# Kernel optimization log

Hardware: AMD Instinct MI355X
Metric: run time of the kernel (lower is better)

## Reference

```python
import math
import jax, jax.numpy as jnp
import numpy as np

B, N, DIM, H = 2, 4096, 1024, 16
DH = DIM // H
LEVELS = int(math.log2(N))
SCALE = 1.0 / math.sqrt(DH)


def build_lookup_table(seq_len):
    """Replicates build_hierarchical_index_lookup_table (numpy, static)."""
    levels = int(math.log2(seq_len))
    total_nodes = 2 * seq_len - 1
    max_valid = total_nodes - 2
    idx = np.full((seq_len, levels), -1, dtype=np.int32)
    cm = np.zeros((seq_len, levels), dtype=bool)
    for n in range(seq_len):
        nc = n
        for l in range(levels):
            if l == 0:
                pair = nc
                nn = nc ^ 1
            else:
                pair = nc // 2 + seq_len
                nn = pair ^ 1  # (nc//2 + seq_len) ^ 1 per Python precedence
            if nn > max_valid:
                break
            if pair < nn:
                cm[n, l] = True  # neighbor is to the right -> causally masked
            idx[n, l] = nn
            nc = nn
    return idx, cm


def setup_inputs() -> dict:
    key = jax.random.key(0)
    ks = jax.random.split(key, 12)
    w = lambda k: (jax.random.normal(k, (DIM, DIM), dtype=jnp.float32) * 0.02)
    idx_np, cm_np = build_lookup_table(N)
    return {
        "x": jax.random.normal(ks[0], (B, N, DIM), dtype=jnp.float32),
        "Wq_y": w(ks[1]), "Wk_y": w(ks[2]), "Wv_y": w(ks[3]),
        "Wo_y": w(ks[4]), "bo_y": jnp.zeros((DIM,), jnp.float32),
        "Wq_x": w(ks[5]), "Wk_x": w(ks[6]), "Wv_x": w(ks[7]),
        "Wo_x": w(ks[8]), "bo_x": jnp.zeros((DIM,), jnp.float32),
        "idx_map": jnp.asarray(idx_np, dtype=jnp.int32),       # [N, LEVELS]
        "causal_mask": jnp.asarray(cm_np, dtype=jnp.bool_),    # [N, LEVELS]
    }


def _heads(t):
    b, n, _ = t.shape
    return t.reshape(b, n, H, DH)


def _forward(x, Wq_y, Wk_y, Wv_y, Wo_y, bo_y, Wq_x, Wk_x, Wv_x, Wo_x, bo_x,
             idx_map, causal_mask):
    # ---- stage 1: build parent nodes level by level (online 2-child softmax merge)
    nodes = [x]  # leaves: [B, N, DIM]; parents appended level by level
    cur = x
    for _ in range(LEVELS):
        pre = 0.5 * (cur[:, 0::2] + cur[:, 1::2])     # parent query source [B,P,DIM]
        q = _heads(pre @ Wq_y)                        # [B,P,H,DH]
        k = _heads(cur @ Wk_y)                        # [B,C,H,DH]
        v = _heads(cur @ Wv_y)
        s0 = jnp.einsum('bphd,bphd->bph', q, k[:, 0::2]) * SCALE
        s1 = jnp.einsum('bphd,bphd->bph', q, k[:, 1::2]) * SCALE
        m = jnp.maximum(s0, s1)
        e0 = jnp.exp(s0 - m)
        e1 = jnp.exp(s1 - m)
        denom = e0 + e1 + 1e-9
        parent = ((e0 / denom)[..., None] * v[:, 0::2]
                  + (e1 / denom)[..., None] * v[:, 1::2])   # [B,P,H,DH]
        bp, pp = parent.shape[0], parent.shape[1]
        parent = parent.reshape(bp, pp, DIM) @ Wo_y + bo_y
        nodes.append(parent)
        cur = parent
    h_all = jnp.concatenate(nodes, axis=1)            # [B, 2N-1, DIM]

    # ---- stage 2: fused multi-level gather attention over self + neighbors
    Q = _heads(x @ Wq_x)                              # leaf queries [B,N,H,DH]
    K_all = _heads(h_all @ Wk_x)                      # [B,2N-1,H,DH]
    V_all = _heads(h_all @ Wv_x)

    k_cross = jnp.take(K_all, idx_map, axis=1)        # [B,N,LEVELS,H,DH]
    v_cross = jnp.take(V_all, idx_map, axis=1)

    s_self = jnp.einsum('bnhd,bnhd->bnh', Q, K_all[:, :N]) * SCALE   # [B,N,H]
    s_cross = jnp.einsum('bnhd,bnlhd->bnhl', Q, k_cross) * SCALE     # [B,N,H,L]
    neg_inf = jnp.float32(-jnp.inf)
    s_cross = jnp.where(causal_mask[None, :, None, :], neg_inf, s_cross)

    scores = jnp.concatenate([s_self[..., None], s_cross], axis=-1)  # [B,N,H,L+1]
    w = jax.nn.softmax(scores, axis=-1)
    out = (w[..., 0:1] * V_all[:, :N]
           + jnp.einsum('bnhl,bnlhd->bnhd', w[..., 1:], v_cross))    # [B,N,H,DH]
    return out.reshape(B, N, DIM) @ Wo_x + bo_x


def reference(x, Wq_y, Wk_y, Wv_y, Wo_y, bo_y, Wq_x, Wk_x, Wv_x, Wo_x, bo_x,
              idx_map, causal_mask):
    return _forward(x, Wq_y, Wk_y, Wv_y, Wo_y, bo_y,
                    Wq_x, Wk_x, Wv_x, Wo_x, bo_x, idx_map, causal_mask)
```

## Files before the change

kernel.cpp:

```cpp
#include <hip/hip_runtime.h>
#include <stdint.h>

#define H_NODES 8191
#define NN 4096
#define DIMC 1024

typedef __bf16 bf16x8 __attribute__((ext_vector_type(8)));
typedef float f32x4 __attribute__((ext_vector_type(4)));

__device__ __forceinline__ float b2f(ushort u) {
  union { uint32_t i; float f; } x; x.i = ((uint32_t)u) << 16; return x.f;
}
__device__ __forceinline__ ushort f2b(float f) {
  union { float f; uint32_t i; } x; x.f = f;
  uint32_t r = x.i + 0x7FFFu + ((x.i >> 16) & 1u);
  return (ushort)(r >> 16);
}
__device__ __forceinline__ void load16f(const ushort* p, float* f) {
  const uint32_t* w = (const uint32_t*)p;
  #pragma unroll
  for (int i = 0; i < 8; ++i) {
    uint32_t v = w[i];
    f[2 * i]     = b2f((ushort)(v & 0xffff));
    f[2 * i + 1] = b2f((ushort)(v >> 16));
  }
}
__device__ __forceinline__ void store16b(ushort* p, const float* f) {
  uint32_t w[8];
  #pragma unroll
  for (int i = 0; i < 8; ++i)
    w[i] = (uint32_t)f2b(f[2 * i]) | ((uint32_t)f2b(f[2 * i + 1]) << 16);
  *(uint4*)p = *(const uint4*)&w[0];
  *(uint4*)(p + 8) = *(const uint4*)&w[4];
}

struct WPtrs { const float* w[8]; };

__global__ void __launch_bounds__(256) transpose_w_k(WPtrs wp, ushort* __restrict__ dst) {
  __shared__ float t[32][33];
  const float* src = wp.w[blockIdx.z];
  int c0 = blockIdx.x * 32, r0 = blockIdx.y * 32;
  int tx = threadIdx.x, ty = threadIdx.y;
  #pragma unroll
  for (int i = ty; i < 32; i += 8)
    t[i][tx] = src[(long)(r0 + i) * DIMC + c0 + tx];
  __syncthreads();
  ushort* d = dst + (long)blockIdx.z * DIMC * DIMC;
  #pragma unroll
  for (int i = ty; i < 32; i += 8)
    d[(long)(c0 + i) * DIMC + r0 + tx] = f2b(t[tx][i]);
}

__global__ void __launch_bounds__(256) cvt_x_k(const float* __restrict__ x, ushort* __restrict__ h) {
  long t = (long)blockIdx.x * 256 + threadIdx.x;
  long i = t << 2;
  if (i >= (long)2 * NN * DIMC) return;
  long row = i >> 10;
  int col = (int)(i & 1023);
  long b = row >> 12;
  long n = row & 4095;
  float4 v = *(const float4*)(x + i);
  ushort* d = h + ((b * H_NODES + n) << 10) + col;
  uint2 pk;
  pk.x = (uint32_t)f2b(v.x) | ((uint32_t)f2b(v.y) << 16);
  pk.y = (uint32_t)f2b(v.z) | ((uint32_t)f2b(v.w) << 16);
  *(uint2*)d = pk;
}

__global__ void __launch_bounds__(256) avg_pairs_k(const ushort* __restrict__ h,
    ushort* __restrict__ pre, int P, int offL) {
  long t = (long)blockIdx.x * 256 + threadIdx.x;
  if (t >= (long)2 * P * 128) return;
  int dblk = (int)(t & 127);
  long r = t >> 7;
  int b = (r >= P) ? 1 : 0;
  int p = (int)(r - (long)b * P);
  const ushort* c = h + (((long)(b * H_NODES + offL + 2 * p)) << 10) + dblk * 8;
  const uint4 a0 = *(const uint4*)c;
  const uint4 a1 = *(const uint4*)(c + DIMC);
  const uint32_t* pa = (const uint32_t*)&a0;
  const uint32_t* pb = (const uint32_t*)&a1;
  uint32_t outw[4];
  #pragma unroll
  for (int i = 0; i < 4; ++i) {
    float x0 = b2f((ushort)(pa[i] & 0xffff)), x1 = b2f((ushort)(pa[i] >> 16));
    float y0 = b2f((ushort)(pb[i] & 0xffff)), y1 = b2f((ushort)(pb[i] >> 16));
    ushort r0 = f2b(0.5f * (x0 + y0)), r1 = f2b(0.5f * (x1 + y1));
    outw[i] = (uint32_t)r0 | ((uint32_t)r1 << 16);
  }
  *(uint4*)(pre + (((long)(b * P + p)) << 10) + dblk * 8) = *(const uint4*)outw;
}

struct GemmDesc {
  const ushort* A; long sAb;
  const ushort* Bt;
  const float* bias;
  void* C; long sCb; int ldc;
  int M; int outMode;
  int tX, tY;
};

__device__ __forceinline__ void stage_tile(const GemmDesc& d, const ushort* Ab,
    int row0, int col0, ushort* lA, ushort* lB, int kt, int wave, int lane) {
  #pragma unroll
  for (int j = 0; j < 2; ++j) {
    int s = wave * 128 + j * 64 + lane;
    int r = s >> 2;
    int g = (s & 3) ^ ((r >> 1) & 3);
    int gr = row0 + r; gr = (gr < d.M) ? gr : (d.M - 1);
    const ushort* srcA = Ab + (long)gr * DIMC + kt * 32 + g * 8;
    __builtin_amdgcn_global_load_lds(
        (const __attribute__((address_space(1))) void*)(uintptr_t)srcA,
        (__attribute__((address_space(3))) void*)(uint32_t)(uintptr_t)(lA + (wave * 128 + j * 64) * 8),
        16, 0, 0);
    const ushort* srcB = d.Bt + (long)(col0 + r) * DIMC + kt * 32 + g * 8;
    __builtin_amdgcn_global_load_lds(
        (const __attribute__((address_space(1))) void*)(uintptr_t)srcB,
        (__attribute__((address_space(3))) void*)(uint32_t)(uintptr_t)(lB + (wave * 128 + j * 64) * 8),
        16, 0, 0);
  }
}

__device__ void gemm_tile(const GemmDesc& d, int bz, int row0, int col0,
    ushort (*lA)[4096], ushort (*lB)[4096], int tid) {
  const ushort* Ab = d.A + (long)bz * d.sAb;
  int wave = tid >> 6, lane = tid & 63;
  int wr = wave >> 1, wc = wave & 1;

  f32x4 acc[4][4];
  #pragma unroll
  for (int m = 0; m < 4; ++m)
    #pragma unroll
    for (int n = 0; n < 4; ++n) acc[m][n] = (f32x4){0.f, 0.f, 0.f, 0.f};

  stage_tile(d, Ab, row0, col0, lA[0], lB[0], 0, wave, lane);
  stage_tile(d, Ab, row0, col0, lA[1], lB[1], 1, wave, lane);
  asm volatile("s_waitcnt vmcnt(4)" ::: "memory");
  __builtin_amdgcn_s_barrier();

  int rr = lane & 15, g4 = lane >> 4;
  for (int kt = 0; kt < 32; ++kt) {
    int cur = kt % 3;
    if (kt + 2 < 32)
      stage_tile(d, Ab, row0, col0, lA[(kt + 2) % 3], lB[(kt + 2) % 3], kt + 2, wave, lane);
    bf16x8 af[4], bfr[4];
    #pragma unroll
    for (int m = 0; m < 4; ++m) {
      int r = wr * 64 + m * 16 + rr;
      int slot = g4 ^ ((r >> 1) & 3);
      af[m] = *reinterpret_cast<const bf16x8*>(&lA[cur][r * 32 + slot * 8]);
    }
    #pragma unroll
    for (int n = 0; n < 4; ++n) {
      int r = wc * 64 + n * 16 + rr;
      int slot = g4 ^ ((r >> 1) & 3);
      bfr[n] = *reinterpret_cast<const bf16x8*>(&lB[cur][r * 32 + slot * 8]);
    }
    __builtin_amdgcn_s_setprio(1);
    #pragma unroll
    for (int m = 0; m < 4; ++m)
      #pragma unroll
      for (int n = 0; n < 4; ++n)
        acc[m][n] = __builtin_amdgcn_mfma_f32_16x16x32_bf16(af[m], bfr[n], acc[m][n], 0, 0, 0);
    __builtin_amdgcn_s_setprio(0);
    if (kt < 30) { asm volatile("s_waitcnt vmcnt(4)" ::: "memory"); }
    else         { asm volatile("s_waitcnt vmcnt(0)" ::: "memory"); }
    if (kt < 31) __builtin_amdgcn_s_barrier();
  }

  int rq = lane >> 4;
  #pragma unroll
  for (int n = 0; n < 4; ++n) {
    int col = col0 + wc * 64 + n * 16 + rr;
    float bv = d.bias ? d.bias[col] : 0.0f;
    #pragma unroll
    for (int m = 0; m < 4; ++m) {
      int gr0 = row0 + wr * 64 + m * 16 + rq * 4;
      #pragma unroll
      for (int r = 0; r < 4; ++r) {
        int gr = gr0 + r;
        if (gr < d.M) {
          float vv = acc[m][n][r] + bv;
          long o = (long)bz * d.sCb + (long)gr * d.ldc + col;
          if (d.outMode == 2) ((float*)d.C)[o] = vv;
          else ((ushort*)d.C)[o] = f2b(vv);
        }
      }
    }
  }
}

__global__ void __launch_bounds__(256) gemm_multi(GemmDesc d0, GemmDesc d1, int t0) {
  __shared__ __align__(16) ushort lA[3][4096];
  __shared__ __align__(16) ushort lB[3][4096];
  int t = blockIdx.x;
  const GemmDesc& d = (t < t0) ? d0 : d1;
  int u = (t < t0) ? t : t - t0;
  int per = d.tX * d.tY;
  int bz = u / per;
  int rem = u - bz * per;
  int ty = rem / d.tX;
  int tx = rem - ty * d.tX;
  gemm_tile(d, bz, tx * 128, ty * 128, lA, lB, threadIdx.x);
}

__global__ void __launch_bounds__(256) merge_y2_k(const ushort* __restrict__ q,
    const ushort* __restrict__ kv, ushort* __restrict__ outp, int P) {
  int wave = threadIdx.x >> 6, lane = threadIdx.x & 63;
  long w = (long)blockIdx.x * 4 + wave;
  if (w >= (long)2 * P) return;
  int b = (w >= P) ? 1 : 0;
  int p = (int)(w - (long)b * P);
  const ushort* qp = q + (((long)(b * P + p)) << 10) + lane * 16;
  const ushort* kvb = kv + ((long)(b * 2 * P + 2 * p)) * 2048;
  float qf[16], k0f[16], k1f[16];
  load16f(qp, qf);
  load16f(kvb + lane * 16, k0f);
  load16f(kvb + 2048 + lane * 16, k1f);
  float d0 = 0.f, d1 = 0.f;
  #pragma unroll
  for (int j = 0; j < 16; ++j) { d0 += qf[j] * k0f[j]; d1 += qf[j] * k1f[j]; }
  d0 += __shfl_xor(d0, 1); d0 += __shfl_xor(d0, 2);
  d1 += __shfl_xor(d1, 1); d1 += __shfl_xor(d1, 2);
  float s0 = d0 * 0.125f, s1 = d1 * 0.125f;
  float mm = fmaxf(s0, s1);
  float e0 = expf(s0 - mm), e1 = expf(s1 - mm);
  float inv = 1.0f / (e0 + e1 + 1e-9f);
  float w0 = e0 * inv, w1 = e1 * inv;
  float v0f[16], v1f[16], ov[16];
  load16f(kvb + 1024 + lane * 16, v0f);
  load16f(kvb + 2048 + 1024 + lane * 16, v1f);
  #pragma unroll
  for (int j = 0; j < 16; ++j) ov[j] = w0 * v0f[j] + w1 * v1f[j];
  store16b(outp + (((long)(b * P + p)) << 10) + lane * 16, ov);
}

__global__ void __launch_bounds__(256) attn_x2_k(const ushort* __restrict__ Q,
    const ushort* __restrict__ KV, ushort* __restrict__ outp) {
  int wave = threadIdx.x >> 6, lane = threadIdx.x & 63;
  long w = (long)blockIdx.x * 4 + wave;
  int n = (int)(w & 4095);
  int b = (int)(w >> 12);
  const ushort* KVb = KV + (long)b * H_NODES * 2048;
  float qf[16];
  load16f(Q + (((long)b * NN + n) << 10) + lane * 16, qf);
  int nb[13];
  nb[0] = n;
  #pragma unroll
  for (int l = 0; l < 12; ++l) nb[1 + l] = (8192 - (8192 >> l)) + ((n >> l) ^ 1);
  float s[13];
  #pragma unroll
  for (int i = 0; i < 13; ++i) {
    float kf[16];
    load16f(KVb + (long)nb[i] * 2048 + lane * 16, kf);
    float d = 0.f;
    #pragma unroll
    for (int j = 0; j < 16; ++j) d += qf[j] * kf[j];
    d += __shfl_xor(d, 1);
    d += __shfl_xor(d, 2);
    s[i] = d * 0.125f;
  }
  #pragma unroll
  for (int l = 0; l < 12; ++l)
    if (((n >> l) & 1) == 0) s[1 + l] = -__builtin_inff();
  float mm = s[0];
  #pragma unroll
  for (int i = 1; i < 13; ++i) mm = fmaxf(mm, s[i]);
  float e[13], sum = 0.f;
  #pragma unroll
  for (int i = 0; i < 13; ++i) { e[i] = expf(s[i] - mm); sum += e[i]; }
  float inv = 1.0f / sum;
  float ov[16];
  #pragma unroll
  for (int j = 0; j < 16; ++j) ov[j] = 0.f;
  #pragma unroll
  for (int i = 0; i < 13; ++i) {
    float wgt = e[i] * inv;
    float vf[16];
    load16f(KVb + (long)nb[i] * 2048 + 1024 + lane * 16, vf);
    #pragma unroll
    for (int j = 0; j < 16; ++j) ov[j] += wgt * vf[j];
  }
  store16b(outp + (((long)b * NN + n) << 10) + lane * 16, ov);
}

extern "C" void kernel_launch(void* const* d_in, const int* in_sizes, int n_in,
                              void* d_out, int out_size, void* d_ws, size_t ws_size,
                              hipStream_t stream) {
  const float* x    = (const float*)d_in[0];
  const float* Wq_y = (const float*)d_in[1];
  const float* Wk_y = (const float*)d_in[2];
  const float* Wv_y = (const float*)d_in[3];
  const float* Wo_y = (const float*)d_in[4];
  const float* bo_y = (const float*)d_in[5];
  const float* Wq_x = (const float*)d_in[6];
  const float* Wk_x = (const float*)d_in[7];
  const float* Wv_x = (const float*)d_in[8];
  const float* Wo_x = (const float*)d_in[9];
  const float* bo_x = (const float*)d_in[10];

  ushort* wt  = (ushort*)d_ws;
  ushort* h   = wt + (size_t)8 * 1024 * 1024;
  ushort* reg = h + (size_t)2 * H_NODES * DIMC;
  ushort* pre = reg;
  ushort* qb  = pre + (size_t)2 * 2048 * DIMC;
  ushort* kv1 = qb  + (size_t)2 * 2048 * DIMC;
  ushort* mrg = kv1 + (size_t)2 * 4096 * 2048;
  ushort* Qx   = reg;
  ushort* KVa  = Qx + (size_t)2 * 4096 * DIMC;
  ushort* aout = KVa + (size_t)2 * H_NODES * 2048;

  size_t need = ((size_t)8 * 1024 * 1024 + (size_t)2 * H_NODES * DIMC +
                 (size_t)2 * 4096 * DIMC + (size_t)2 * H_NODES * 2048 +
                 (size_t)2 * 4096 * DIMC) * 2;
  if (ws_size < need) return;

  WPtrs wp;
  wp.w[0] = Wq_y; wp.w[1] = Wk_y; wp.w[2] = Wv_y; wp.w[3] = Wo_y;
  wp.w[4] = Wq_x; wp.w[5] = Wk_x; wp.w[6] = Wv_x; wp.w[7] = Wo_x;
  transpose_w_k<<<dim3(32, 32, 8), dim3(32, 8), 0, stream>>>(wp, wt);
  cvt_x_k<<<8192, 256, 0, stream>>>(x, h);

  auto mkdesc = [](const ushort* A, long sAb, const ushort* Bt, const float* bias,
                   void* C, long sCb, int ldc, int M, int outMode, int tY) {
    GemmDesc d; d.A = A; d.sAb = sAb; d.Bt = Bt; d.bias = bias; d.C = C; d.sCb = sCb;
    d.ldc = ldc; d.M = M; d.outMode = outMode; d.tX = (M + 127) / 128; d.tY = tY;
    return d;
  };

  for (int l = 0; l < 12; ++l) {
    int C = NN >> l, P = C >> 1;
    int offL = 8192 - (8192 >> l);
    int offP = 8192 - (8192 >> (l + 1));
    avg_pairs_k<<<(2 * P * 128 + 255) / 256, 256, 0, stream>>>(h, pre, P, offL);
    GemmDesc dq = mkdesc(pre, (long)P * DIMC, wt, nullptr,
                         qb, (long)P * DIMC, DIMC, P, 0, 8);
    GemmDesc dkv = mkdesc(h + (long)offL * DIMC, (long)H_NODES * DIMC,
                          wt + (size_t)1 * 1024 * 1024, nullptr,
                          kv1, (long)C * 2048, 2048, C, 0, 16);
    int t0 = dq.tX * dq.tY * 2, t1 = dkv.tX * dkv.tY * 2;
    gemm_multi<<<t0 + t1, 256, 0, stream>>>(dq, dkv, t0);
    merge_y2_k<<<(2 * P + 3) / 4, 256, 0, stream>>>(qb, kv1, mrg, P);
    GemmDesc dgo = mkdesc(mrg, (long)P * DIMC, wt + (size_t)3 * 1024 * 1024, bo_y,
                          h + (long)offP * DIMC, (long)H_NODES * DIMC, DIMC, P, 1, 8);
    gemm_multi<<<dgo.tX * dgo.tY * 2, 256, 0, stream>>>(dgo, dgo, dgo.tX * dgo.tY * 2);
  }

  GemmDesc dqx = mkdesc(h, (long)H_NODES * DIMC, wt + (size_t)4 * 1024 * 1024, nullptr,
                        Qx, (long)4096 * DIMC, DIMC, 4096, 0, 8);
  GemmDesc dkva = mkdesc(h, (long)H_NODES * DIMC, wt + (size_t)5 * 1024 * 1024, nullptr,
                         KVa, (long)H_NODES * 2048, 2048, H_NODES, 0, 16);
  int t0 = dqx.tX * dqx.tY * 2, t1 = dkva.tX * dkva.tY * 2;
  gemm_multi<<<t0 + t1, 256, 0, stream>>>(dqx, dkva, t0);
  attn_x2_k<<<2048, 256, 0, stream>>>(Qx, KVa, aout);
  GemmDesc dox = mkdesc(aout, (long)4096 * DIMC, wt + (size_t)7 * 1024 * 1024, bo_x,
                        d_out, (long)4096 * DIMC, DIMC, 4096, 2, 8);
  gemm_multi<<<dox.tX * dox.tY * 2, 256, 0, stream>>>(dox, dox, dox.tX * dox.tY * 2);
}
```

Before: 784.4 us.

## Add 256x256-tile GEMM kernel with direct-to-LDS loads for large GEMMs

Adds a new 512-thread GEMM kernel that computes 256x256 output tiles. It stages A and B through global_load_lds with an XOR-swizzled LDS layout, double buffers with half-tile prefetch interleaved across four compute phases, and raises wave priority around the MFMA blocks. The kernel replaces the 128x128 path for the large tree levels and for the final Q/KV/output projections. The larger tiles are meant to raise arithmetic intensity and reduce global and LDS traffic per FLOP. In exchange they produce fewer blocks, which can underfill the CUs, and they use 128KB of LDS per block.

Result: slower. 949.0 us (+21.0%).

```diff
diff --git a/kernel.cpp b/kernel.cpp
--- a/kernel.cpp
+++ b/kernel.cpp
@@ -204,6 +204,143 @@
   gemm_tile(d, bz, tx * 128, ty * 128, lA, lB, threadIdx.x);
 }
 
+__device__ __forceinline__ void stage_half256(const ushort* gbase, int maxRow,
+    ushort* ldsbase, int tid) {
+  #pragma unroll
+  for (int L = 0; L < 2; ++L) {
+    int s = L * 512 + tid;
+    int lrow = s >> 3, b = s & 7;
+    int gb = b ^ ((lrow >> 1) & 7);
+    int er = lrow < maxRow ? lrow : maxRow - 1;
+    const ushort* src = gbase + (long)er * DIMC + gb * 8;
+    __builtin_amdgcn_global_load_lds(
+        (const __attribute__((address_space(1))) void*)(uintptr_t)src,
+        (__attribute__((address_space(3))) void*)(uint32_t)(uintptr_t)(ldsbase + s * 8),
+        16, 0, 0);
+  }
+}
+
+__global__ void __launch_bounds__(512, 2) gemm256_multi(GemmDesc d0, GemmDesc d1, int t0full) {
+  __shared__ __align__(16) ushort smem[65536];
+  int t = blockIdx.x;
+  const GemmDesc& d = (t < t0full) ? d0 : d1;
+  int u = (t < t0full) ? t : t - t0full;
+  int per = d.tX * d.tY;
+  int bz = u / per;
+  int rem = u - bz * per;
+  int ty = rem / d.tX;
+  int tx = rem - ty * d.tX;
+  int row0 = tx * 256, col0 = ty * 256;
+  const ushort* Ab = d.A + (long)bz * d.sAb;
+  const ushort* Bt = d.Bt;
+
+  int tid = threadIdx.x;
+  int wave = tid >> 6, lane = tid & 63;
+  int wm = wave >> 2, wn = wave & 3;
+  int rr = lane & 15, g = lane >> 4;
+  int qrr = (rr >> 1) & 7;
+  int pb0 = (g ^ qrr) * 8;
+  int pb1 = ((4 + g) ^ qrr) * 8;
+
+  auto stA = [&](int tile, int half) {
+    const ushort* gbp = Ab + (long)(row0 + half * 128) * DIMC + tile * 64;
+    int maxR = d.M - row0 - half * 128;
+    stage_half256(gbp, maxR, smem + (tile & 1) * 16384 + half * 8192, tid);
+  };
+  auto stB = [&](int tile, int half) {
+    const ushort* gbp = Bt + (long)(col0 + half * 128) * DIMC + tile * 64;
+    stage_half256(gbp, 1 << 28, smem + 32768 + (tile & 1) * 16384 + half * 8192, tid);
+  };
+
+  f32x4 acc[2][2][4][2];
+  #pragma unroll
+  for (int a0 = 0; a0 < 2; ++a0)
+    #pragma unroll
+    for (int a1 = 0; a1 < 2; ++a1)
+      #pragma unroll
+      for (int a2 = 0; a2 < 4; ++a2)
+        #pragma unroll
+        for (int a3 = 0; a3 < 2; ++a3)
+          acc[a0][a1][a2][a3] = (f32x4){0.f, 0.f, 0.f, 0.f};
+
+  stA(0, 0); stA(0, 1); stB(0, 0); stB(0, 1);
+  stA(1, 0); stB(1, 0);
+  asm volatile("s_waitcnt vmcnt(4)" ::: "memory");
+  __builtin_amdgcn_s_barrier();
+
+  for (int kt = 0; kt < 16; ++kt) {
+    ushort* aCur = smem + (kt & 1) * 16384;
+    ushort* bCur = smem + 32768 + (kt & 1) * 16384;
+    #pragma unroll
+    for (int ph = 0; ph < 4; ++ph) {
+      const int qm = ph >> 1, qn = ph & 1;
+      ushort* aH = aCur + qm * 8192;
+      ushort* bH = bCur + qn * 8192;
+      bf16x8 af[4][2], bfr[2][2];
+      #pragma unroll
+      for (int m = 0; m < 4; ++m) {
+        int lr = (wm * 64 + m * 16 + rr) * 64;
+        af[m][0] = *reinterpret_cast<const bf16x8*>(aH + lr + pb0);
+        af[m][1] = *reinterpret_cast<const bf16x8*>(aH + lr + pb1);
+      }
+      #pragma unroll
+      for (int n = 0; n < 2; ++n) {
+        int lr = (wn * 32 + n * 16 + rr) * 64;
+        bfr[n][0] = *reinterpret_cast<const bf16x8*>(bH + lr + pb0);
+        bfr[n][1] = *reinterpret_cast<const bf16x8*>(bH + lr + pb1);
+      }
+      if (ph == 0 && kt + 1 < 16) stA(kt + 1, 1);
+      if (ph == 1 && kt + 1 < 16) stB(kt + 1, 1);
+      if (ph == 2 && kt + 2 < 16) stA(kt + 2, 0);
+      if (ph == 3 && kt + 2 < 16) stB(kt + 2, 0);
+      asm volatile("" ::: "memory");
+      __builtin_amdgcn_s_barrier();
+      asm volatile("s_waitcnt lgkmcnt(0)" ::: "memory");
+      __builtin_amdgcn_s_setprio(1);
+      #pragma unroll
+      for (int m = 0; m < 4; ++m)
+        #pragma unroll
+        for (int n = 0; n < 2; ++n)
+          #pragma unroll
+          for (int ks = 0; ks < 2; ++ks)
+            acc[qm][qn][m][n] = __builtin_amdgcn_mfma_f32_16x16x32_bf16(
+                af[m][ks], bfr[n][ks], acc[qm][qn][m][n], 0, 0, 0);
+      __builtin_amdgcn_s_setprio(0);
+      if (ph == 3) {
+        if (kt + 2 < 16) { asm volatile("s_waitcnt vmcnt(4)" ::: "memory"); }
+        else             { asm volatile("s_waitcnt vmcnt(0)" ::: "memory"); }
+      }
+      asm volatile("" ::: "memory");
+      __builtin_amdgcn_s_barrier();
+    }
+  }
+
+  int rq = lane >> 4;
+  #pragma unroll
+  for (int qn = 0; qn < 2; ++qn)
+    #pragma unroll
+    for (int n = 0; n < 2; ++n) {
+      int col = col0 + qn * 128 + wn * 32 + n * 16 + rr;
+      float bv = d.bias ? d.bias[col] : 0.0f;
+      #pragma unroll
+      for (int qm = 0; qm < 2; ++qm)
+        #pragma unroll
+        for (int m = 0; m < 4; ++m) {
+          int gr0 = row0 + qm * 128 + wm * 64 + m * 16 + rq * 4;
+          #pragma unroll
+          for (int r = 0; r < 4; ++r) {
+            int gr = gr0 + r;
+            if (gr < d.M) {
+              float vv = acc[qm][qn][m][n][r] + bv;
+              long o = (long)bz * d.sCb + (long)gr * d.ldc + col;
+              if (d.outMode == 2) ((float*)d.C)[o] = vv;
+              else ((ushort*)d.C)[o] = f2b(vv);
+            }
+          }
+        }
+    }
+}
+
 __global__ void __launch_bounds__(256) merge_y2_k(const ushort* __restrict__ q,
     const ushort* __restrict__ kv, ushort* __restrict__ outp, int P) {
   int wave = threadIdx.x >> 6, lane = threadIdx.x & 63;
@@ -321,10 +458,16 @@
   transpose_w_k<<<dim3(32, 32, 8), dim3(32, 8), 0, stream>>>(wp, wt);
   cvt_x_k<<<8192, 256, 0, stream>>>(x, h);
 
-  auto mkdesc = [](const ushort* A, long sAb, const ushort* Bt, const float* bias,
-                   void* C, long sCb, int ldc, int M, int outMode, int tY) {
+  auto mk128 = [](const ushort* A, long sAb, const ushort* Bt, const float* bias,
+                  void* C, long sCb, int ldc, int M, int outMode, int tY) {
     GemmDesc d; d.A = A; d.sAb = sAb; d.Bt = Bt; d.bias = bias; d.C = C; d.sCb = sCb;
     d.ldc = ldc; d.M = M; d.outMode = outMode; d.tX = (M + 127) / 128; d.tY = tY;
+    return d;
+  };
+  auto mk256 = [](const ushort* A, long sAb, const ushort* Bt, const float* bias,
+                  void* C, long sCb, int ldc, int M, int outMode, int tY) {
+    GemmDesc d; d.A = A; d.sAb = sAb; d.Bt = Bt; d.bias = bias; d.C = C; d.sCb = sCb;
+    d.ldc = ldc; d.M = M; d.outMode = outMode; d.tX = (M + 255) / 256; d.tY = tY;
     return d;
   };
 
@@ -333,27 +476,43 @@
     int offL = 8192 - (8192 >> l);
     int offP = 8192 - (8192 >> (l + 1));
     avg_pairs_k<<<(2 * P * 128 + 255) / 256, 256, 0, stream>>>(h, pre, P, offL);
-    GemmDesc dq = mkdesc(pre, (long)P * DIMC, wt, nullptr,
-                         qb, (long)P * DIMC, DIMC, P, 0, 8);
-    GemmDesc dkv = mkdesc(h + (long)offL * DIMC, (long)H_NODES * DIMC,
-                          wt + (size_t)1 * 1024 * 1024, nullptr,
-                          kv1, (long)C * 2048, 2048, C, 0, 16);
-    int t0 = dq.tX * dq.tY * 2, t1 = dkv.tX * dkv.tY * 2;
-    gemm_multi<<<t0 + t1, 256, 0, stream>>>(dq, dkv, t0);
+    if (l <= 2) {
+      GemmDesc dq = mk256(pre, (long)P * DIMC, wt, nullptr,
+                          qb, (long)P * DIMC, DIMC, P, 0, 4);
+      GemmDesc dkv = mk256(h + (long)offL * DIMC, (long)H_NODES * DIMC,
+                           wt + (size_t)1 * 1024 * 1024, nullptr,
+                           kv1, (long)C * 2048, 2048, C, 0, 8);
+      int t0 = dq.tX * dq.tY * 2, t1 = dkv.tX * dkv.tY * 2;
+      gemm256_multi<<<t0 + t1, 512, 0, stream>>>(dq, dkv, t0);
+    } else {
+      GemmDesc dq = mk128(pre, (long)P * DIMC, wt, nullptr,
+                          qb, (long)P * DIMC, DIMC, P, 0, 8);
+      GemmDesc dkv = mk128(h + (long)offL * DIMC, (long)H_NODES * DIMC,
+                           wt + (size_t)1 * 1024 * 1024, nullptr,
+                           kv1, (long)C * 2048, 2048, C, 0, 16);
+      int t0 = dq.tX * dq.tY * 2, t1 = dkv.tX * dkv.tY * 2;
+      gemm_multi<<<t0 + t1, 256, 0, stream>>>(dq, dkv, t0);
+    }
     merge_y2_k<<<(2 * P + 3) / 4, 256, 0, stream>>>(qb, kv1, mrg, P);
-    GemmDesc dgo = mkdesc(mrg, (long)P * DIMC, wt + (size_t)3 * 1024 * 1024, bo_y,
-                          h + (long)offP * DIMC, (long)H_NODES * DIMC, DIMC, P, 1, 8);
-    gemm_multi<<<dgo.tX * dgo.tY * 2, 256, 0, stream>>>(dgo, dgo, dgo.tX * dgo.tY * 2);
-  }
-
-  GemmDesc dqx = mkdesc(h, (long)H_NODES * DIMC, wt + (size_t)4 * 1024 * 1024, nullptr,
-                        Qx, (long)4096 * DIMC, DIMC, 4096, 0, 8);
-  GemmDesc dkva = mkdesc(h, (long)H_NODES * DIMC, wt + (size_t)5 * 1024 * 1024, nullptr,
-                         KVa, (long)H_NODES * 2048, 2048, H_NODES, 0, 16);
+    if (P >= 1024) {
+      GemmDesc dgo = mk256(mrg, (long)P * DIMC, wt + (size_t)3 * 1024 * 1024, bo_y,
+                           h + (long)offP * DIMC, (long)H_NODES * DIMC, DIMC, P, 1, 4);
+      gemm256_multi<<<dgo.tX * dgo.tY * 2, 512, 0, stream>>>(dgo, dgo, dgo.tX * dgo.tY * 2);
+    } else {
+      GemmDesc dgo = mk128(mrg, (long)P * DIMC, wt + (size_t)3 * 1024 * 1024, bo_y,
+                           h + (long)offP * DIMC, (long)H_NODES * DIMC, DIMC, P, 1, 8);
+      gemm_multi<<<dgo.tX * dgo.tY * 2, 256, 0, stream>>>(dgo, dgo, dgo.tX * dgo.tY * 2);
+    }
+  }
+
+  GemmDesc dqx = mk256(h, (long)H_NODES * DIMC, wt + (size_t)4 * 1024 * 1024, nullptr,
+                       Qx, (long)4096 * DIMC, DIMC, 4096, 0, 4);
+  GemmDesc dkva = mk256(h, (long)H_NODES * DIMC, wt + (size_t)5 * 1024 * 1024, nullptr,
+                        KVa, (long)H_NODES * 2048, 2048, H_NODES, 0, 8);
   int t0 = dqx.tX * dqx.tY * 2, t1 = dkva.tX * dkva.tY * 2;
-  gemm_multi<<<t0 + t1, 256, 0, stream>>>(dqx, dkva, t0);
+  gemm256_multi<<<t0 + t1, 512, 0, stream>>>(dqx, dkva, t0);
   attn_x2_k<<<2048, 256, 0, stream>>>(Qx, KVa, aout);
-  GemmDesc dox = mkdesc(aout, (long)4096 * DIMC, wt + (size_t)7 * 1024 * 1024, bo_x,
-                        d_out, (long)4096 * DIMC, DIMC, 4096, 2, 8);
-  gemm_multi<<<dox.tX * dox.tY * 2, 256, 0, stream>>>(dox, dox, dox.tX * dox.tY * 2);
-}
+  GemmDesc dox = mk256(aout, (long)4096 * DIMC, wt + (size_t)7 * 1024 * 1024, bo_x,
+                       d_out, (long)4096 * DIMC, DIMC, 4096, 2, 4);
+  gemm256_multi<<<dox.tX * dox.tY * 2, 512, 0, stream>>>(dox, dox, dox.tX * dox.tY * 2);
+}
```

## Backfill small tree-level GEMM launches with final Qx/KV projection tiles

Applied to the files above, without the earlier changes.

Adds a scheduler kernel that pads each small per-level GEMM launch (levels 3 and up) with tiles of the final x-attention Q and K/V projections. A KV tile is only issued once the tree rows it reads have already been written. The goal is to fill idle compute units during the tiny late-level launches and shrink the large final projection GEMM. To make this possible, the small-level scratch buffers move into the aout region so they cannot overlap Qx and KVa, and KV tiles use a row-major ordering so they follow tree-row availability. The price is more complex indexing and longer, mixed-work launches on the sequential level chain.

Measured after the change: 1.041 ms. 32.7% more time.

```diff
diff --git a/kernel.cpp b/kernel.cpp
--- a/kernel.cpp
+++ b/kernel.cpp
@@ -121,7 +121,7 @@
   }
 }
 
-__device__ void gemm_tile(const GemmDesc& d, int bz, int row0, int col0,
+__device__ __forceinline__ void gemm_tile(const GemmDesc& d, int bz, int row0, int col0,
     ushort (*lA)[4096], ushort (*lB)[4096], int tid) {
   const ushort* Ab = d.A + (long)bz * d.sAb;
   int wave = tid >> 6, lane = tid & 63;
@@ -190,18 +190,32 @@
   }
 }
 
-__global__ void __launch_bounds__(256) gemm_multi(GemmDesc d0, GemmDesc d1, int t0) {
+struct SchedArgs {
+  GemmDesc r0, r1, q, kv;
+  int n0, n1;
+  int qOff, qCnt;
+  int kvOff;
+};
+
+__global__ void __launch_bounds__(256) gemm_sched_k(SchedArgs s) {
   __shared__ __align__(16) ushort lA[3][4096];
   __shared__ __align__(16) ushort lB[3][4096];
   int t = blockIdx.x;
-  const GemmDesc& d = (t < t0) ? d0 : d1;
-  int u = (t < t0) ? t : t - t0;
-  int per = d.tX * d.tY;
-  int bz = u / per;
-  int rem = u - bz * per;
-  int ty = rem / d.tX;
-  int tx = rem - ty * d.tX;
-  gemm_tile(d, bz, tx * 128, ty * 128, lA, lB, threadIdx.x);
+  const GemmDesc* d;
+  int idx, ord = 0;
+  if (t < s.n0) { d = &s.r0; idx = t; }
+  else if (t < s.n0 + s.n1) { d = &s.r1; idx = t - s.n0; }
+  else if (t < s.n0 + s.n1 + s.qCnt) { d = &s.q; idx = s.qOff + (t - s.n0 - s.n1); }
+  else { d = &s.kv; idx = s.kvOff + (t - s.n0 - s.n1 - s.qCnt); ord = 1; }
+  int bz, tx, ty;
+  if (ord) {
+    tx = idx >> 5; int r = idx & 31; ty = r >> 1; bz = r & 1;
+  } else {
+    int per = d->tX * d->tY;
+    bz = idx / per; int rem = idx - bz * per;
+    ty = rem / d->tX; tx = rem - ty * d->tX;
+  }
+  gemm_tile(*d, bz, tx * 128, ty * 128, lA, lB, threadIdx.x);
 }
 
 __global__ void __launch_bounds__(256) merge_y2_k(const ushort* __restrict__ q,
@@ -302,13 +316,17 @@
   ushort* wt  = (ushort*)d_ws;
   ushort* h   = wt + (size_t)8 * 1024 * 1024;
   ushort* reg = h + (size_t)2 * H_NODES * DIMC;
-  ushort* pre = reg;
-  ushort* qb  = pre + (size_t)2 * 2048 * DIMC;
-  ushort* kv1 = qb  + (size_t)2 * 2048 * DIMC;
-  ushort* mrg = kv1 + (size_t)2 * 4096 * 2048;
   ushort* Qx   = reg;
   ushort* KVa  = Qx + (size_t)2 * 4096 * DIMC;
   ushort* aout = KVa + (size_t)2 * H_NODES * 2048;
+  ushort* preB = reg;
+  ushort* qbB  = preB + (size_t)2 * 2048 * DIMC;
+  ushort* kv1B = qbB + (size_t)2 * 2048 * DIMC;
+  ushort* mrgB = kv1B + (size_t)2 * 4096 * 2048;
+  ushort* preS = aout;
+  ushort* qbS  = preS + (size_t)2 * 256 * DIMC;
+  ushort* kv1S = qbS + (size_t)2 * 256 * DIMC;
+  ushort* mrgS = kv1S + (size_t)2 * 512 * 2048;
 
   size_t need = ((size_t)8 * 1024 * 1024 + (size_t)2 * H_NODES * DIMC +
                  (size_t)2 * 4096 * DIMC + (size_t)2 * H_NODES * 2048 +
@@ -321,39 +339,71 @@
   transpose_w_k<<<dim3(32, 32, 8), dim3(32, 8), 0, stream>>>(wp, wt);
   cvt_x_k<<<8192, 256, 0, stream>>>(x, h);
 
-  auto mkdesc = [](const ushort* A, long sAb, const ushort* Bt, const float* bias,
-                   void* C, long sCb, int ldc, int M, int outMode, int tY) {
+  auto mk128 = [](const ushort* A, long sAb, const ushort* Bt, const float* bias,
+                  void* C, long sCb, int ldc, int M, int outMode, int tY) {
     GemmDesc d; d.A = A; d.sAb = sAb; d.Bt = Bt; d.bias = bias; d.C = C; d.sCb = sCb;
     d.ldc = ldc; d.M = M; d.outMode = outMode; d.tX = (M + 127) / 128; d.tY = tY;
     return d;
   };
 
+  GemmDesc dQat = mk128(h, (long)H_NODES * DIMC, wt + (size_t)4 * 1024 * 1024, nullptr,
+                        Qx, (long)4096 * DIMC, DIMC, 4096, 0, 8);
+  GemmDesc dKat = mk128(h, (long)H_NODES * DIMC, wt + (size_t)5 * 1024 * 1024, nullptr,
+                        KVa, (long)H_NODES * 2048, 2048, H_NODES, 0, 16);
+  const int QTOT = 512, KVTOT = 2048, RATION = 160;
+  int qCur = 0, kvCur = 0;
+
+  auto sched = [&](GemmDesc r0, int n0, GemmDesc r1, int n1, int l) {
+    int aq = 0, akv = 0;
+    if (l >= 3) {
+      int cap = 512 - (n0 + n1);
+      if (cap > RATION) cap = RATION;
+      if (cap < 0) cap = 0;
+      int kvLimit = ((8192 - (8192 >> (l + 1))) >> 7) * 32;
+      if (kvLimit > KVTOT) kvLimit = KVTOT;
+      aq = QTOT - qCur; if (aq > cap) aq = cap;
+      akv = kvLimit - kvCur; if (akv > cap - aq) akv = cap - aq; if (akv < 0) akv = 0;
+    }
+    SchedArgs s; s.r0 = r0; s.r1 = r1; s.q = dQat; s.kv = dKat;
+    s.n0 = n0; s.n1 = n1; s.qOff = qCur; s.qCnt = aq; s.kvOff = kvCur;
+    gemm_sched_k<<<n0 + n1 + aq + akv, 256, 0, stream>>>(s);
+    qCur += aq; kvCur += akv;
+  };
+
   for (int l = 0; l < 12; ++l) {
-    int C = NN >> l, P = C >> 1;
+    int P = NN >> (l + 1);
     int offL = 8192 - (8192 >> l);
     int offP = 8192 - (8192 >> (l + 1));
+    bool small = (l >= 3);
+    ushort* pre = small ? preS : preB;
+    ushort* qb  = small ? qbS  : qbB;
+    ushort* kv1 = small ? kv1S : kv1B;
+    ushort* mrg = small ? mrgS : mrgB;
     avg_pairs_k<<<(2 * P * 128 + 255) / 256, 256, 0, stream>>>(h, pre, P, offL);
-    GemmDesc dq = mkdesc(pre, (long)P * DIMC, wt, nullptr,
+    GemmDesc dq  = mk128(pre, (long)P * DIMC, wt, nullptr,
                          qb, (long)P * DIMC, DIMC, P, 0, 8);
-    GemmDesc dkv = mkdesc(h + (long)offL * DIMC, (long)H_NODES * DIMC,
-                          wt + (size_t)1 * 1024 * 1024, nullptr,
-                          kv1, (long)C * 2048, 2048, C, 0, 16);
-    int t0 = dq.tX * dq.tY * 2, t1 = dkv.tX * dkv.tY * 2;
-    gemm_multi<<<t0 + t1, 256, 0, stream>>>(dq, dkv, t0);
+    GemmDesc dkv = mk128(h + (long)offL * DIMC, (long)H_NODES * DIMC,
+                         wt + (size_t)1 * 1024 * 1024, nullptr,
+                         kv1, (long)2 * P * 2048, 2048, 2 * P, 0, 16);
+    sched(dq, dq.tX * dq.tY * 2, dkv, dkv.tX * dkv.tY * 2, l);
     merge_y2_k<<<(2 * P + 3) / 4, 256, 0, stream>>>(qb, kv1, mrg, P);
-    GemmDesc dgo = mkdesc(mrg, (long)P * DIMC, wt + (size_t)3 * 1024 * 1024, bo_y,
-                          h + (long)offP * DIMC, (long)H_NODES * DIMC, DIMC, P, 1, 8);
-    gemm_multi<<<dgo.tX * dgo.tY * 2, 256, 0, stream>>>(dgo, dgo, dgo.tX * dgo.tY * 2);
-  }
-
-  GemmDesc dqx = mkdesc(h, (long)H_NODES * DIMC, wt + (size_t)4 * 1024 * 1024, nullptr,
-                        Qx, (long)4096 * DIMC, DIMC, 4096, 0, 8);
-  GemmDesc dkva = mkdesc(h, (long)H_NODES * DIMC, wt + (size_t)5 * 1024 * 1024, nullptr,
-                         KVa, (long)H_NODES * 2048, 2048, H_NODES, 0, 16);
-  int t0 = dqx.tX * dqx.tY * 2, t1 = dkva.tX * dkva.tY * 2;
-  gemm_multi<<<t0 + t1, 256, 0, stream>>>(dqx, dkva, t0);
+    GemmDesc dgo = mk128(mrg, (long)P * DIMC, wt + (size_t)3 * 1024 * 1024, bo_y,
+                         h + (long)offP * DIMC, (long)H_NODES * DIMC, DIMC, P, 1, 8);
+    sched(dgo, dgo.tX * dgo.tY * 2, dgo, 0, l);
+  }
+
+  {
+    SchedArgs s; s.r0 = dQat; s.n0 = 0; s.r1 = dQat; s.n1 = 0; s.q = dQat; s.kv = dKat;
+    s.qOff = qCur; s.qCnt = QTOT - qCur; s.kvOff = kvCur;
+    int grid = s.qCnt + (KVTOT - kvCur);
+    if (grid > 0) gemm_sched_k<<<grid, 256, 0, stream>>>(s);
+  }
   attn_x2_k<<<2048, 256, 0, stream>>>(Qx, KVa, aout);
-  GemmDesc dox = mkdesc(aout, (long)4096 * DIMC, wt + (size_t)7 * 1024 * 1024, bo_x,
-                        d_out, (long)4096 * DIMC, DIMC, 4096, 2, 8);
-  gemm_multi<<<dox.tX * dox.tY * 2, 256, 0, stream>>>(dox, dox, dox.tX * dox.tY * 2);
-}
+  {
+    GemmDesc dox = mk128(aout, (long)4096 * DIMC, wt + (size_t)7 * 1024 * 1024, bo_x,
+                         d_out, (long)4096 * DIMC, DIMC, 4096, 2, 8);
+    SchedArgs s; s.r0 = dox; s.n0 = dox.tX * dox.tY * 2; s.r1 = dox; s.n1 = 0;
+    s.q = dQat; s.kv = dKat; s.qOff = 0; s.qCnt = 0; s.kvOff = 0;
+    gemm_sched_k<<<s.n0, 256, 0, stream>>>(s);
+  }
+}
```

## Fuse pair-averaging into output GEMM epilogue and overlap final projections with tree levels

Applied to the files above, without the earlier changes.

The output-projection GEMM epilogue now also writes the averaged parent-query input for the next level, so the per-level avg_pairs kernel launch goes away. The stage-2 K/V and Q projections over already-finished tree nodes are split into chunks and issued in the same grid as the small late-level GEMMs. That fills otherwise idle compute units and cuts the number of launches. Small-level scratch buffers are moved into the aout region to avoid aliasing with KVa/Qx, which makes the buffer layout more fragile.

New measurement: 661.3 us. -15.7%, faster.

```diff
diff --git a/kernel.cpp b/kernel.cpp
--- a/kernel.cpp
+++ b/kernel.cpp
@@ -98,6 +98,8 @@
   void* C; long sCb; int ldc;
   int M; int outMode;
   int tX, tY;
+  ushort* preC;
+  long sPreB;
 };
 
 __device__ __forceinline__ void stage_tile(const GemmDesc& d, const ushort* Ab,
@@ -121,7 +123,7 @@
   }
 }
 
-__device__ void gemm_tile(const GemmDesc& d, int bz, int row0, int col0,
+__device__ __forceinline__ void gemm_tile(const GemmDesc& d, int bz, int row0, int col0,
     ushort (*lA)[4096], ushort (*lB)[4096], int tid) {
   const ushort* Ab = d.A + (long)bz * d.sAb;
   int wave = tid >> 6, lane = tid & 63;
@@ -176,14 +178,25 @@
     #pragma unroll
     for (int m = 0; m < 4; ++m) {
       int gr0 = row0 + wr * 64 + m * 16 + rq * 4;
+      float vv[4];
+      #pragma unroll
+      for (int r = 0; r < 4; ++r) vv[r] = acc[m][n][r] + bv;
       #pragma unroll
       for (int r = 0; r < 4; ++r) {
         int gr = gr0 + r;
         if (gr < d.M) {
-          float vv = acc[m][n][r] + bv;
           long o = (long)bz * d.sCb + (long)gr * d.ldc + col;
-          if (d.outMode == 2) ((float*)d.C)[o] = vv;
-          else ((ushort*)d.C)[o] = f2b(vv);
+          if (d.outMode == 2) ((float*)d.C)[o] = vv[r];
+          else ((ushort*)d.C)[o] = f2b(vv[r]);
+        }
+      }
+      if (d.preC) {
+        #pragma unroll
+        for (int r = 0; r < 4; r += 2) {
+          int gr = gr0 + r;
+          if (gr + 1 < d.M)
+            d.preC[(long)bz * d.sPreB + (long)(gr >> 1) * DIMC + col] =
+                f2b(0.5f * (vv[r] + vv[r + 1]));
         }
       }
     }
@@ -302,13 +315,17 @@
   ushort* wt  = (ushort*)d_ws;
   ushort* h   = wt + (size_t)8 * 1024 * 1024;
   ushort* reg = h + (size_t)2 * H_NODES * DIMC;
-  ushort* pre = reg;
-  ushort* qb  = pre + (size_t)2 * 2048 * DIMC;
-  ushort* kv1 = qb  + (size_t)2 * 2048 * DIMC;
-  ushort* mrg = kv1 + (size_t)2 * 4096 * 2048;
   ushort* Qx   = reg;
   ushort* KVa  = Qx + (size_t)2 * 4096 * DIMC;
   ushort* aout = KVa + (size_t)2 * H_NODES * 2048;
+  ushort* preB = reg;
+  ushort* qbB  = preB + (size_t)2 * 2048 * DIMC;
+  ushort* kv1B = qbB + (size_t)2 * 2048 * DIMC;
+  ushort* mrgB = kv1B + (size_t)2 * 4096 * 2048;
+  ushort* preS = aout;
+  ushort* qbS  = preS + (size_t)2 * 256 * DIMC;
+  ushort* kv1S = qbS + (size_t)2 * 256 * DIMC;
+  ushort* mrgS = kv1S + (size_t)2 * 512 * 2048;
 
   size_t need = ((size_t)8 * 1024 * 1024 + (size_t)2 * H_NODES * DIMC +
                  (size_t)2 * 4096 * DIMC + (size_t)2 * H_NODES * 2048 +
@@ -320,40 +337,69 @@
   wp.w[4] = Wq_x; wp.w[5] = Wk_x; wp.w[6] = Wv_x; wp.w[7] = Wo_x;
   transpose_w_k<<<dim3(32, 32, 8), dim3(32, 8), 0, stream>>>(wp, wt);
   cvt_x_k<<<8192, 256, 0, stream>>>(x, h);
-
-  auto mkdesc = [](const ushort* A, long sAb, const ushort* Bt, const float* bias,
-                   void* C, long sCb, int ldc, int M, int outMode, int tY) {
+  avg_pairs_k<<<(2 * 2048 * 128 + 255) / 256, 256, 0, stream>>>(h, preB, 2048, 0);
+
+  auto mk128 = [](const ushort* A, long sAb, const ushort* Bt, const float* bias,
+                  void* C, long sCb, int ldc, int M, int outMode, int tY) {
     GemmDesc d; d.A = A; d.sAb = sAb; d.Bt = Bt; d.bias = bias; d.C = C; d.sCb = sCb;
     d.ldc = ldc; d.M = M; d.outMode = outMode; d.tX = (M + 127) / 128; d.tY = tY;
+    d.preC = nullptr; d.sPreB = 0;
     return d;
   };
+  auto kvSub = [&](long start, int len) {
+    return mk128(h + start * DIMC, (long)H_NODES * DIMC, wt + (size_t)5 * 1024 * 1024,
+                 nullptr, KVa + start * 2048, (long)H_NODES * 2048, 2048, len, 0, 16);
+  };
 
   for (int l = 0; l < 12; ++l) {
-    int C = NN >> l, P = C >> 1;
+    int P = NN >> (l + 1);
     int offL = 8192 - (8192 >> l);
     int offP = 8192 - (8192 >> (l + 1));
-    avg_pairs_k<<<(2 * P * 128 + 255) / 256, 256, 0, stream>>>(h, pre, P, offL);
-    GemmDesc dq = mkdesc(pre, (long)P * DIMC, wt, nullptr,
+    bool small = (l >= 3);
+    ushort* pre = small ? preS : preB;
+    ushort* qb  = small ? qbS  : qbB;
+    ushort* kv1 = small ? kv1S : kv1B;
+    ushort* mrg = small ? mrgS : mrgB;
+
+    GemmDesc dq  = mk128(pre, (long)P * DIMC, wt, nullptr,
                          qb, (long)P * DIMC, DIMC, P, 0, 8);
-    GemmDesc dkv = mkdesc(h + (long)offL * DIMC, (long)H_NODES * DIMC,
-                          wt + (size_t)1 * 1024 * 1024, nullptr,
-                          kv1, (long)C * 2048, 2048, C, 0, 16);
-    int t0 = dq.tX * dq.tY * 2, t1 = dkv.tX * dkv.tY * 2;
-    gemm_multi<<<t0 + t1, 256, 0, stream>>>(dq, dkv, t0);
+    GemmDesc dkv = mk128(h + (long)offL * DIMC, (long)H_NODES * DIMC,
+                         wt + (size_t)1 * 1024 * 1024, nullptr,
+                         kv1, (long)2 * P * 2048, 2048, 2 * P, 0, 16);
+    int t0 = dq.tX * dq.tY * 2;
+    gemm_multi<<<t0 + dkv.tX * dkv.tY * 2, 256, 0, stream>>>(dq, dkv, t0);
+
     merge_y2_k<<<(2 * P + 3) / 4, 256, 0, stream>>>(qb, kv1, mrg, P);
-    GemmDesc dgo = mkdesc(mrg, (long)P * DIMC, wt + (size_t)3 * 1024 * 1024, bo_y,
-                          h + (long)offP * DIMC, (long)H_NODES * DIMC, DIMC, P, 1, 8);
-    gemm_multi<<<dgo.tX * dgo.tY * 2, 256, 0, stream>>>(dgo, dgo, dgo.tX * dgo.tY * 2);
-  }
-
-  GemmDesc dqx = mkdesc(h, (long)H_NODES * DIMC, wt + (size_t)4 * 1024 * 1024, nullptr,
-                        Qx, (long)4096 * DIMC, DIMC, 4096, 0, 8);
-  GemmDesc dkva = mkdesc(h, (long)H_NODES * DIMC, wt + (size_t)5 * 1024 * 1024, nullptr,
-                         KVa, (long)H_NODES * 2048, 2048, H_NODES, 0, 16);
-  int t0 = dqx.tX * dqx.tY * 2, t1 = dkva.tX * dkva.tY * 2;
-  gemm_multi<<<t0 + t1, 256, 0, stream>>>(dqx, dkva, t0);
+
+    GemmDesc dgo = mk128(mrg, (long)P * DIMC, wt + (size_t)3 * 1024 * 1024, bo_y,
+                         h + (long)offP * DIMC, (long)H_NODES * DIMC, DIMC, P, 1, 8);
+    if (l < 11) {
+      dgo.preC = (l >= 2) ? preS : preB;
+      dgo.sPreB = (long)(P / 2) * DIMC;
+    }
+    GemmDesc att = dgo; int nAtt = 0;
+    if (l == 4)      { att = kvSub(0, 2048); }
+    else if (l == 5) { att = kvSub(2048, 2048); }
+    else if (l == 6) { att = kvSub(4096, 2048); }
+    else if (l == 7) { att = kvSub(6144, 1792); }
+    else if (l == 8) { att = kvSub(7936, 240); }
+    else if (l == 9) { att = mk128(h, (long)H_NODES * DIMC, wt + (size_t)4 * 1024 * 1024,
+                                   nullptr, Qx, (long)4096 * DIMC, DIMC, 4096, 0, 8); }
+    else if (l == 10) { att = kvSub(8176, 12); }
+    else if (l == 11) { att = kvSub(8188, 2); }
+    if (l >= 4) nAtt = att.tX * att.tY * 2;
+    int n0 = dgo.tX * dgo.tY * 2;
+    gemm_multi<<<n0 + nAtt, 256, 0, stream>>>(dgo, att, n0);
+  }
+
+  {
+    GemmDesc att = kvSub(8190, 1);
+    gemm_multi<<<att.tX * att.tY * 2, 256, 0, stream>>>(att, att, att.tX * att.tY * 2);
+  }
   attn_x2_k<<<2048, 256, 0, stream>>>(Qx, KVa, aout);
-  GemmDesc dox = mkdesc(aout, (long)4096 * DIMC, wt + (size_t)7 * 1024 * 1024, bo_x,
-                        d_out, (long)4096 * DIMC, DIMC, 4096, 2, 8);
-  gemm_multi<<<dox.tX * dox.tY * 2, 256, 0, stream>>>(dox, dox, dox.tX * dox.tY * 2);
-}
+  {
+    GemmDesc dox = mk128(aout, (long)4096 * DIMC, wt + (size_t)7 * 1024 * 1024, bo_x,
+                         d_out, (long)4096 * DIMC, DIMC, 4096, 2, 8);
+    gemm_multi<<<dox.tX * dox.tY * 2, 256, 0, stream>>>(dox, dox, dox.tX * dox.tY * 2);
+  }
+}
```
